# Performance work log

Measured on AMD Instinct MI355X. Metric: run time of the kernel, lower is better.

Reference implementation:

```python
import jax, jax.numpy as jnp
import numpy as np

B, T, C = 4, 2048, 1024
H = 16
HD = C // H  # 64


def setup_inputs() -> dict:
    key = jax.random.key(0)
    k1, k2, k3 = jax.random.split(key, 3)
    x = jax.random.normal(k1, (B, T, C), dtype=jnp.float32)
    W_attn = jax.random.normal(k2, (C, 3 * C), dtype=jnp.float32) * (1.0 / np.sqrt(C))
    b_attn = jnp.zeros((3 * C,), dtype=jnp.float32)
    W_proj = jax.random.normal(k3, (C, C), dtype=jnp.float32) * (1.0 / np.sqrt(C))
    b_proj = jnp.zeros((C,), dtype=jnp.float32)
    return {"x": x, "W_attn": W_attn, "b_attn": b_attn, "W_proj": W_proj, "b_proj": b_proj}


def reference(x, W_attn, b_attn, W_proj, b_proj):
    Bx, Tx, Cx = x.shape
    qkv = x @ W_attn + b_attn                      # [B,T,3C]
    q, k, v = jnp.split(qkv, 3, axis=-1)
    # [B,T,C] -> [B,H,T,HD]
    q = q.reshape(Bx, Tx, H, HD).transpose(0, 2, 1, 3)
    k = k.reshape(Bx, Tx, H, HD).transpose(0, 2, 1, 3)
    v = v.reshape(Bx, Tx, H, HD).transpose(0, 2, 1, 3)
    att = jnp.einsum('bhqd,bhkd->bhqk', q, k) / jnp.sqrt(jnp.float32(HD))
    causal = jnp.tril(jnp.ones((Tx, Tx), dtype=bool))
    att = jnp.where(causal[None, None], att, -jnp.inf)
    att = jax.nn.softmax(att, axis=-1)
    y = jnp.einsum('bhqk,bhkd->bhqd', att, v)      # [B,H,T,HD]
    y = y.transpose(0, 2, 1, 3).reshape(Bx, Tx, Cx)
    return y @ W_proj + b_proj
```

## Files before the change

kernel.cpp:

```cpp
#include <hip/hip_runtime.h>
#include <hip/hip_bf16.h>

typedef unsigned short u16;
typedef __attribute__((ext_vector_type(8))) short bf16x8;
typedef __attribute__((ext_vector_type(4))) float f32x4;

#define MFMA16(a, b, c) __builtin_amdgcn_mfma_f32_16x16x32_bf16((a), (b), (c), 0, 0, 0)

__device__ __forceinline__ u16 f2bf(float f) {
  union { float f; unsigned u; } v; v.f = f;
  unsigned r = v.u + 0x7fffu + ((v.u >> 16) & 1u);
  return (u16)(r >> 16);
}

__device__ __forceinline__ unsigned pk_trunc(float hi, float lo) {
  union { float f; unsigned u; } a, b; a.f = hi; b.f = lo;
  return __builtin_amdgcn_perm(a.u, b.u, 0x07060302u);
}

__device__ __forceinline__ void gload_lds16(const u16* g, u16* l) {
  __builtin_amdgcn_global_load_lds((const __attribute__((address_space(1))) void*)g,
                                   (__attribute__((address_space(3))) void*)l, 16, 0, 0);
}

__global__ __launch_bounds__(256) void convert_bf16_k(const float* __restrict__ in,
                                                      u16* __restrict__ out, int n) {
  int i = (blockIdx.x * 256 + threadIdx.x) * 4;
  if (i >= n) return;
  float4 v = *(const float4*)(in + i);
  ushort4 o;
  o.x = f2bf(v.x); o.y = f2bf(v.y); o.z = f2bf(v.z); o.w = f2bf(v.w);
  *(ushort4*)(out + i) = o;
}

__global__ __launch_bounds__(256) void transpose_bf16_k(const float* __restrict__ W,
                                                        u16* __restrict__ Wt, int K, int N) {
  __shared__ float tile[64][65];
  const int n0 = blockIdx.x * 64, k0 = blockIdx.y * 64;
  const int tx = threadIdx.x & 63, ty = threadIdx.x >> 6;
#pragma unroll
  for (int i = 0; i < 16; ++i)
    tile[ty + 4 * i][tx] = W[(size_t)(k0 + ty + 4 * i) * N + n0 + tx];
  __syncthreads();
#pragma unroll
  for (int i = 0; i < 16; ++i)
    Wt[(size_t)(n0 + ty + 4 * i) * K + k0 + tx] = f2bf(tile[tx][ty + 4 * i]);
}

#define GEMM_CORE(Aptr, Btptr)                                                     \
  __shared__ u16 As[128 * 32];                                                     \
  __shared__ u16 Bs[128 * 32];                                                     \
  const int m0 = blockIdx.y * 128, n0 = blockIdx.x * 128;                          \
  const int tid = threadIdx.x;                                                     \
  const int w = tid >> 6, lane = tid & 63;                                         \
  const int wm = w & 1, wn = w >> 1;                                               \
  const int fr = lane & 15, fg = lane >> 4;                                        \
  const int srow = lane >> 2, skof = (lane & 3) * 8;                               \
  const u16* gA0 = (Aptr) + (size_t)(m0 + w * 32 + srow) * 1024 + skof;            \
  const u16* gB0 = (Btptr) + (size_t)(n0 + w * 32 + srow) * 1024 + skof;           \
  u16* lA = As + w * 1024;                                                         \
  u16* lB = Bs + w * 1024;                                                         \
  f32x4 acc[4][4];                                                                 \
  _Pragma("unroll") for (int i = 0; i < 4; i++)                                    \
      _Pragma("unroll") for (int j = 0; j < 4; j++) acc[i][j] = (f32x4){0, 0, 0, 0}; \
  for (int kt = 0; kt < 32; ++kt) {                                                \
    const int ko = kt * 32;                                                        \
    gload_lds16(gA0 + ko, lA);                                                     \
    gload_lds16(gA0 + ko + 16 * 1024, lA + 512);                                   \
    gload_lds16(gB0 + ko, lB);                                                     \
    gload_lds16(gB0 + ko + 16 * 1024, lB + 512);                                   \
    __syncthreads();                                                               \
    bf16x8 af[4], bfr[4];                                                          \
    _Pragma("unroll") for (int mb = 0; mb < 4; ++mb)                               \
        af[mb] = *(const bf16x8*)&As[(wm * 64 + mb * 16 + fr) * 32 + fg * 8];      \
    _Pragma("unroll") for (int nb = 0; nb < 4; ++nb)                               \
        bfr[nb] = *(const bf16x8*)&Bs[(wn * 64 + nb * 16 + fr) * 32 + fg * 8];     \
    _Pragma("unroll") for (int mb = 0; mb < 4; ++mb)                               \
        _Pragma("unroll") for (int nb = 0; nb < 4; ++nb)                           \
            acc[mb][nb] = MFMA16(af[mb], bfr[nb], acc[mb][nb]);                    \
    __syncthreads();                                                               \
  }

__global__ __launch_bounds__(256) void gemm_qkv(const u16* __restrict__ A,
                                                const u16* __restrict__ Bt,
                                                const float* __restrict__ bias,
                                                u16* __restrict__ Qo, u16* __restrict__ Ko,
                                                u16* __restrict__ Vt) {
  GEMM_CORE(A, Bt)
  const int which = n0 >> 10;
#pragma unroll
  for (int nb = 0; nb < 4; ++nb) {
    const int n = n0 + wn * 64 + nb * 16 + fr;
    const float bs = bias[n];
    const int c = n & 1023, h = c >> 6, hd = c & 63;
#pragma unroll
    for (int mb = 0; mb < 4; ++mb) {
      const int mbase = m0 + wm * 64 + mb * 16 + fg * 4;
      const int bb = mbase >> 11;
      const int t = mbase & 2047;
      if (which == 0) {
        u16* dst = Qo + ((size_t)(bb * 16 + h) * 2048 + t) * 64 + hd;
#pragma unroll
        for (int r = 0; r < 4; ++r) dst[(size_t)r * 64] = f2bf((acc[mb][nb][r] + bs) * 0.125f);
      } else if (which == 1) {
        u16* dst = Ko + ((size_t)(bb * 16 + h) * 2048 + t) * 64 + hd;
#pragma unroll
        for (int r = 0; r < 4; ++r) dst[(size_t)r * 64] = f2bf(acc[mb][nb][r] + bs);
      } else {
        ushort4 pv;
        pv.x = f2bf(acc[mb][nb][0] + bs);
        pv.y = f2bf(acc[mb][nb][1] + bs);
        pv.z = f2bf(acc[mb][nb][2] + bs);
        pv.w = f2bf(acc[mb][nb][3] + bs);
        *(ushort4*)(Vt + ((size_t)(bb * 16 + h) * 64 + hd) * 2048 + t) = pv;
      }
    }
  }
}

__global__ __launch_bounds__(256) void gemm_proj(const u16* __restrict__ A,
                                                 const u16* __restrict__ Bt,
                                                 const float* __restrict__ bias,
                                                 float* __restrict__ O) {
  GEMM_CORE(A, Bt)
#pragma unroll
  for (int nb = 0; nb < 4; ++nb) {
    const int n = n0 + wn * 64 + nb * 16 + fr;
    const float bs = bias[n];
#pragma unroll
    for (int mb = 0; mb < 4; ++mb) {
#pragma unroll
      for (int r = 0; r < 4; ++r) {
        const int m = m0 + wm * 64 + mb * 16 + fg * 4 + r;
        O[(size_t)m * 1024 + n] = acc[mb][nb][r] + bs;
      }
    }
  }
}

#define PSTR 88
__global__ __launch_bounds__(256) void attn_k(const u16* __restrict__ Q,
                                              const u16* __restrict__ Kb,
                                              const u16* __restrict__ Vt,
                                              u16* __restrict__ Y) {
  __shared__ u16 Ks[64 * 72];
  __shared__ u16 Vs[64 * 72];
  __shared__ u16 Ps[4 * 32 * PSTR];
  const int L = blockIdx.x;
  const int xcd = L & 7, slot = L >> 3;
  const int bh = xcd * 8 + (slot & 7);
  const int qt = 15 - (slot >> 3);
  const int tid = threadIdx.x, w = tid >> 6, lane = tid & 63;
  const int fr = lane & 15, fg = lane >> 4;
  const u16* Qp = Q + (size_t)bh * 2048 * 64;
  const u16* Kp = Kb + (size_t)bh * 2048 * 64;
  const u16* Vp = Vt + (size_t)bh * 64 * 2048;
  const int qw = qt * 128 + w * 32;

  bf16x8 qa[2][2];
#pragma unroll
  for (int g = 0; g < 2; ++g)
#pragma unroll
    for (int c = 0; c < 2; ++c)
      qa[g][c] = *(const bf16x8*)(Qp + (size_t)(qw + g * 16 + fr) * 64 + c * 32 + fg * 8);

  float li[2] = {0.f, 0.f};
  f32x4 ot[2][4];
#pragma unroll
  for (int g = 0; g < 2; ++g)
#pragma unroll
    for (int mb = 0; mb < 4; ++mb) ot[g][mb] = (f32x4){0, 0, 0, 0};

  const int srow = tid >> 2, scol = (tid & 3) * 16;
  u16* Pw = Ps + w * 32 * PSTR;
  const int nk = 2 * qt + 2;
  const u16* Kg = Kp + (size_t)srow * 64 + scol;
  const u16* Vg = Vp + (size_t)srow * 2048 + scol;

  uint4 kr0 = *(const uint4*)(Kg);
  uint4 kr1 = *(const uint4*)(Kg + 8);
  uint4 vr0 = *(const uint4*)(Vg);
  uint4 vr1 = *(const uint4*)(Vg + 8);

  for (int jt = 0; jt < nk; ++jt) {
    const int k0 = jt * 64;
    if (jt) __syncthreads();
    *(uint4*)&Ks[srow * 72 + scol] = kr0;
    *(uint4*)&Ks[srow * 72 + scol + 8] = kr1;
    *(uint4*)&Vs[srow * 72 + scol] = vr0;
    *(uint4*)&Vs[srow * 72 + scol + 8] = vr1;
    __syncthreads();
    if (jt + 1 < nk) {
      const int kn = (jt + 1) * 64;
      kr0 = *(const uint4*)(Kg + (size_t)kn * 64);
      kr1 = *(const uint4*)(Kg + (size_t)kn * 64 + 8);
      vr0 = *(const uint4*)(Vg + kn);
      vr1 = *(const uint4*)(Vg + kn + 8);
    }
    if (k0 > qw + 31) continue;

    bf16x8 kb[4][2];
#pragma unroll
    for (int nb = 0; nb < 4; ++nb) {
      kb[nb][0] = *(const bf16x8*)&Ks[(nb * 16 + fr) * 72 + fg * 8];
      kb[nb][1] = *(const bf16x8*)&Ks[(nb * 16 + fr) * 72 + 32 + fg * 8];
    }
    f32x4 st[2][4];
#pragma unroll
    for (int g = 0; g < 2; ++g)
#pragma unroll
      for (int nb = 0; nb < 4; ++nb) {
        f32x4 z = (f32x4){0, 0, 0, 0};
        z = MFMA16(kb[nb][0], qa[g][0], z);
        z = MFMA16(kb[nb][1], qa[g][1], z);
        st[g][nb] = z;
      }
    const bool needmask = (k0 + 63 > qw);
#pragma unroll
    for (int g = 0; g < 2; ++g) {
      const int q = qw + g * 16 + fr;
      float rs0 = 0.f, rs1 = 0.f;
#pragma unroll
      for (int nb = 0; nb < 4; ++nb) {
        const int kcb = k0 + nb * 16 + 4 * fg;
        float p0 = __expf(st[g][nb][0]);
        float p1 = __expf(st[g][nb][1]);
        float p2 = __expf(st[g][nb][2]);
        float p3 = __expf(st[g][nb][3]);
        if (needmask) {
          p0 = (kcb + 0 > q) ? 0.f : p0;
          p1 = (kcb + 1 > q) ? 0.f : p1;
          p2 = (kcb + 2 > q) ? 0.f : p2;
          p3 = (kcb + 3 > q) ? 0.f : p3;
        }
        rs0 += p0 + p1;
        rs1 += p2 + p3;
        *(uint2*)&Pw[(g * 16 + fr) * PSTR + nb * 16 + 4 * fg] =
            make_uint2(pk_trunc(p1, p0), pk_trunc(p3, p2));
      }
      li[g] += rs0 + rs1;
    }
    bf16x8 pa[2][2];
#pragma unroll
    for (int g = 0; g < 2; ++g)
#pragma unroll
      for (int H = 0; H < 2; ++H)
        pa[g][H] = *(const bf16x8*)&Pw[(g * 16 + fr) * PSTR + H * 32 + fg * 8];
#pragma unroll
    for (int mb = 0; mb < 4; ++mb) {
      bf16x8 vb0 = *(const bf16x8*)&Vs[(mb * 16 + fr) * 72 + fg * 8];
      bf16x8 vb1 = *(const bf16x8*)&Vs[(mb * 16 + fr) * 72 + 32 + fg * 8];
#pragma unroll
      for (int g = 0; g < 2; ++g) {
        ot[g][mb] = MFMA16(vb0, pa[g][0], ot[g][mb]);
        ot[g][mb] = MFMA16(vb1, pa[g][1], ot[g][mb]);
      }
    }
  }

  const int b = bh >> 4, h = bh & 15;
#pragma unroll
  for (int g = 0; g < 2; ++g) {
    float l = li[g];
    l += __shfl_xor(l, 16);
    l += __shfl_xor(l, 32);
    const float inv = 1.0f / l;
    const int t = qw + g * 16 + fr;
    u16* yrow = Y + ((size_t)b * 2048 + t) * 1024 + h * 64;
#pragma unroll
    for (int mb = 0; mb < 4; ++mb) {
      const unsigned d0 = (unsigned)f2bf(ot[g][mb][0] * inv) |
                          ((unsigned)f2bf(ot[g][mb][1] * inv) << 16);
      const unsigned d1 = (unsigned)f2bf(ot[g][mb][2] * inv) |
                          ((unsigned)f2bf(ot[g][mb][3] * inv) << 16);
      *(uint2*)&yrow[mb * 16 + fg * 4] = make_uint2(d0, d1);
    }
  }
}

extern "C" void kernel_launch(void* const* d_in, const int* in_sizes, int n_in,
                              void* d_out, int out_size, void* d_ws, size_t ws_size,
                              hipStream_t stream) {
  const float* x = (const float*)d_in[0];
  const float* Wa = (const float*)d_in[1];
  const float* ba = (const float*)d_in[2];
  const float* Wp = (const float*)d_in[3];
  const float* bp = (const float*)d_in[4];
  float* out = (float*)d_out;

  char* p = (char*)d_ws;
  u16* xb = (u16*)p;   p += (size_t)8192 * 1024 * 2;
  u16* WaT = (u16*)p;  p += (size_t)3072 * 1024 * 2;
  u16* WpT = (u16*)p;  p += (size_t)1024 * 1024 * 2;
  u16* Qb = (u16*)p;   p += (size_t)64 * 2048 * 64 * 2;
  u16* Kbuf = (u16*)p; p += (size_t)64 * 2048 * 64 * 2;
  u16* Vtb = (u16*)p;  p += (size_t)64 * 64 * 2048 * 2;
  u16* Yb = (u16*)p;   p += (size_t)8192 * 1024 * 2;

  convert_bf16_k<<<8192, 256, 0, stream>>>(x, xb, 8192 * 1024);
  transpose_bf16_k<<<dim3(48, 16), 256, 0, stream>>>(Wa, WaT, 1024, 3072);
  transpose_bf16_k<<<dim3(16, 16), 256, 0, stream>>>(Wp, WpT, 1024, 1024);
  gemm_qkv<<<dim3(24, 64), 256, 0, stream>>>(xb, WaT, ba, Qb, Kbuf, Vtb);
  attn_k<<<1024, 256, 0, stream>>>(Qb, Kbuf, Vtb, Yb);
  gemm_proj<<<dim3(8, 64), 256, 0, stream>>>(Yb, WpT, bp, out);
}
```

Baseline: 270.9 us.

## Swap MFMA operands for row-vectorized GEMM epilogues, merge weight transposes, remap blocks

Merges the two weight-transpose launches into one kernel. Swaps the MFMA operand order in the Q/K and projection GEMMs so each lane holds four consecutive columns, which lets the epilogue write packed 8-byte bf16 or 16-byte float4 stores instead of scattered 2- or 4-byte stores. Remaps the 1D block index so consecutive blocks share an M tile and are spread across XCDs for better L2 reuse. It also changes the attention P-buffer stride from 88 to 72, which may introduce LDS bank conflicts.

```diff
diff --git a/kernel.cpp b/kernel.cpp
--- a/kernel.cpp
+++ b/kernel.cpp
@@ -33,10 +33,13 @@
   *(ushort4*)(out + i) = o;
 }
 
-__global__ __launch_bounds__(256) void transpose_bf16_k(const float* __restrict__ W,
-                                                        u16* __restrict__ Wt, int K, int N) {
+__global__ __launch_bounds__(256) void transpose2_k(const float* __restrict__ Wa, u16* __restrict__ WaT,
+                                                    const float* __restrict__ Wp, u16* __restrict__ WpT) {
   __shared__ float tile[64][65];
-  const int n0 = blockIdx.x * 64, k0 = blockIdx.y * 64;
+  int b = blockIdx.x;
+  const float* W; u16* Wt; int N, n0, k0;
+  if (b < 768) { W = Wa; Wt = WaT; N = 3072; n0 = (b % 48) * 64; k0 = (b / 48) * 64; }
+  else { int c = b - 768; W = Wp; Wt = WpT; N = 1024; n0 = (c & 15) * 64; k0 = (c >> 4) * 64; }
   const int tx = threadIdx.x & 63, ty = threadIdx.x >> 6;
 #pragma unroll
   for (int i = 0; i < 16; ++i)
@@ -44,41 +47,45 @@
   __syncthreads();
 #pragma unroll
   for (int i = 0; i < 16; ++i)
-    Wt[(size_t)(n0 + ty + 4 * i) * K + k0 + tx] = f2bf(tile[tx][ty + 4 * i]);
-}
-
-#define GEMM_CORE(Aptr, Btptr)                                                     \
+    Wt[(size_t)(n0 + ty + 4 * i) * 1024 + k0 + tx] = f2bf(tile[tx][ty + 4 * i]);
+}
+
+#define GEMM_PROLOG                                                                \
   __shared__ u16 As[128 * 32];                                                     \
   __shared__ u16 Bs[128 * 32];                                                     \
-  const int m0 = blockIdx.y * 128, n0 = blockIdx.x * 128;                          \
   const int tid = threadIdx.x;                                                     \
   const int w = tid >> 6, lane = tid & 63;                                         \
   const int wm = w & 1, wn = w >> 1;                                               \
   const int fr = lane & 15, fg = lane >> 4;                                        \
   const int srow = lane >> 2, skof = (lane & 3) * 8;                               \
-  const u16* gA0 = (Aptr) + (size_t)(m0 + w * 32 + srow) * 1024 + skof;            \
-  const u16* gB0 = (Btptr) + (size_t)(n0 + w * 32 + srow) * 1024 + skof;           \
   u16* lA = As + w * 1024;                                                         \
   u16* lB = Bs + w * 1024;                                                         \
   f32x4 acc[4][4];                                                                 \
   _Pragma("unroll") for (int i = 0; i < 4; i++)                                    \
-      _Pragma("unroll") for (int j = 0; j < 4; j++) acc[i][j] = (f32x4){0, 0, 0, 0}; \
-  for (int kt = 0; kt < 32; ++kt) {                                                \
-    const int ko = kt * 32;                                                        \
-    gload_lds16(gA0 + ko, lA);                                                     \
-    gload_lds16(gA0 + ko + 16 * 1024, lA + 512);                                   \
-    gload_lds16(gB0 + ko, lB);                                                     \
-    gload_lds16(gB0 + ko + 16 * 1024, lB + 512);                                   \
-    __syncthreads();                                                               \
-    bf16x8 af[4], bfr[4];                                                          \
-    _Pragma("unroll") for (int mb = 0; mb < 4; ++mb)                               \
-        af[mb] = *(const bf16x8*)&As[(wm * 64 + mb * 16 + fr) * 32 + fg * 8];      \
-    _Pragma("unroll") for (int nb = 0; nb < 4; ++nb)                               \
-        bfr[nb] = *(const bf16x8*)&Bs[(wn * 64 + nb * 16 + fr) * 32 + fg * 8];     \
-    _Pragma("unroll") for (int mb = 0; mb < 4; ++mb)                               \
-        _Pragma("unroll") for (int nb = 0; nb < 4; ++nb)                           \
-            acc[mb][nb] = MFMA16(af[mb], bfr[nb], acc[mb][nb]);                    \
-    __syncthreads();                                                               \
+      _Pragma("unroll") for (int j = 0; j < 4; j++) acc[i][j] = (f32x4){0, 0, 0, 0};
+
+#define GEMM_KLOOP(Aptr, Btptr, SWAP)                                              \
+  {                                                                                \
+    const u16* gA0 = (Aptr) + (size_t)(m0 + w * 32 + srow) * 1024 + skof;          \
+    const u16* gB0 = (Btptr) + (size_t)(n0 + w * 32 + srow) * 1024 + skof;         \
+    for (int kt = 0; kt < 32; ++kt) {                                              \
+      const int ko = kt * 32;                                                      \
+      gload_lds16(gA0 + ko, lA);                                                   \
+      gload_lds16(gA0 + ko + 16 * 1024, lA + 512);                                 \
+      gload_lds16(gB0 + ko, lB);                                                   \
+      gload_lds16(gB0 + ko + 16 * 1024, lB + 512);                                 \
+      __syncthreads();                                                             \
+      bf16x8 af[4], bfr[4];                                                        \
+      _Pragma("unroll") for (int mb = 0; mb < 4; ++mb)                             \
+          af[mb] = *(const bf16x8*)&As[(wm * 64 + mb * 16 + fr) * 32 + fg * 8];    \
+      _Pragma("unroll") for (int nb = 0; nb < 4; ++nb)                             \
+          bfr[nb] = *(const bf16x8*)&Bs[(wn * 64 + nb * 16 + fr) * 32 + fg * 8];   \
+      _Pragma("unroll") for (int mb = 0; mb < 4; ++mb)                             \
+          _Pragma("unroll") for (int nb = 0; nb < 4; ++nb)                         \
+              acc[mb][nb] = (SWAP) ? MFMA16(bfr[nb], af[mb], acc[mb][nb])          \
+                                   : MFMA16(af[mb], bfr[nb], acc[mb][nb]);         \
+      __syncthreads();                                                             \
+    }                                                                              \
   }
 
 __global__ __launch_bounds__(256) void gemm_qkv(const u16* __restrict__ A,
@@ -86,27 +93,46 @@
                                                 const float* __restrict__ bias,
                                                 u16* __restrict__ Qo, u16* __restrict__ Ko,
                                                 u16* __restrict__ Vt) {
-  GEMM_CORE(A, Bt)
+  const int id = blockIdx.x;
+  const int s = id >> 3;
+  const int nt = (id & 7) * 3 + s % 3;
+  const int mt = s / 3;
+  const int m0 = mt * 128, n0 = nt * 128;
+  GEMM_PROLOG
   const int which = n0 >> 10;
-#pragma unroll
-  for (int nb = 0; nb < 4; ++nb) {
-    const int n = n0 + wn * 64 + nb * 16 + fr;
-    const float bs = bias[n];
-    const int c = n & 1023, h = c >> 6, hd = c & 63;
+  if (which < 2) {
+    GEMM_KLOOP(A, Bt, 1)
+    const float sc = (which == 0) ? 0.125f : 1.0f;
+    u16* Out = (which == 0) ? Qo : Ko;
 #pragma unroll
     for (int mb = 0; mb < 4; ++mb) {
-      const int mbase = m0 + wm * 64 + mb * 16 + fg * 4;
-      const int bb = mbase >> 11;
-      const int t = mbase & 2047;
-      if (which == 0) {
-        u16* dst = Qo + ((size_t)(bb * 16 + h) * 2048 + t) * 64 + hd;
-#pragma unroll
-        for (int r = 0; r < 4; ++r) dst[(size_t)r * 64] = f2bf((acc[mb][nb][r] + bs) * 0.125f);
-      } else if (which == 1) {
-        u16* dst = Ko + ((size_t)(bb * 16 + h) * 2048 + t) * 64 + hd;
-#pragma unroll
-        for (int r = 0; r < 4; ++r) dst[(size_t)r * 64] = f2bf(acc[mb][nb][r] + bs);
-      } else {
+      const int tg = m0 + wm * 64 + mb * 16 + fr;
+      const int bb = tg >> 11, t = tg & 2047;
+#pragma unroll
+      for (int nb = 0; nb < 4; ++nb) {
+        const int n = n0 + wn * 64 + nb * 16 + 4 * fg;
+        const float4 b4 = *(const float4*)(bias + n);
+        const int c = n & 1023, h = c >> 6, d0 = c & 63;
+        const float v0 = (acc[mb][nb][0] + b4.x) * sc;
+        const float v1 = (acc[mb][nb][1] + b4.y) * sc;
+        const float v2 = (acc[mb][nb][2] + b4.z) * sc;
+        const float v3 = (acc[mb][nb][3] + b4.w) * sc;
+        const unsigned lo = (unsigned)f2bf(v0) | ((unsigned)f2bf(v1) << 16);
+        const unsigned hi = (unsigned)f2bf(v2) | ((unsigned)f2bf(v3) << 16);
+        *(uint2*)(Out + ((size_t)(bb * 16 + h) * 2048 + t) * 64 + d0) = make_uint2(lo, hi);
+      }
+    }
+  } else {
+    GEMM_KLOOP(A, Bt, 0)
+#pragma unroll
+    for (int nb = 0; nb < 4; ++nb) {
+      const int n = n0 + wn * 64 + nb * 16 + fr;
+      const float bs = bias[n];
+      const int c = n & 1023, h = c >> 6, hd = c & 63;
+#pragma unroll
+      for (int mb = 0; mb < 4; ++mb) {
+        const int mbase = m0 + wm * 64 + mb * 16 + fg * 4;
+        const int bb = mbase >> 11, t = mbase & 2047;
         ushort4 pv;
         pv.x = f2bf(acc[mb][nb][0] + bs);
         pv.y = f2bf(acc[mb][nb][1] + bs);
@@ -122,23 +148,28 @@
                                                  const u16* __restrict__ Bt,
                                                  const float* __restrict__ bias,
                                                  float* __restrict__ O) {
-  GEMM_CORE(A, Bt)
-#pragma unroll
-  for (int nb = 0; nb < 4; ++nb) {
-    const int n = n0 + wn * 64 + nb * 16 + fr;
-    const float bs = bias[n];
-#pragma unroll
-    for (int mb = 0; mb < 4; ++mb) {
-#pragma unroll
-      for (int r = 0; r < 4; ++r) {
-        const int m = m0 + wm * 64 + mb * 16 + fg * 4 + r;
-        O[(size_t)m * 1024 + n] = acc[mb][nb][r] + bs;
-      }
-    }
-  }
-}
-
-#define PSTR 88
+  const int id = blockIdx.x;
+  const int m0 = (id >> 3) * 128, n0 = (id & 7) * 128;
+  GEMM_PROLOG
+  GEMM_KLOOP(A, Bt, 1)
+#pragma unroll
+  for (int mb = 0; mb < 4; ++mb) {
+    const int tg = m0 + wm * 64 + mb * 16 + fr;
+#pragma unroll
+    for (int nb = 0; nb < 4; ++nb) {
+      const int n = n0 + wn * 64 + nb * 16 + 4 * fg;
+      const float4 b4 = *(const float4*)(bias + n);
+      float4 o;
+      o.x = acc[mb][nb][0] + b4.x;
+      o.y = acc[mb][nb][1] + b4.y;
+      o.z = acc[mb][nb][2] + b4.z;
+      o.w = acc[mb][nb][3] + b4.w;
+      *(float4*)(O + (size_t)tg * 1024 + n) = o;
+    }
+  }
+}
+
+#define PSTR 72
 __global__ __launch_bounds__(256) void attn_k(const u16* __restrict__ Q,
                                               const u16* __restrict__ Kb,
                                               const u16* __restrict__ Vt,
@@ -298,9 +329,8 @@
   u16* Yb = (u16*)p;   p += (size_t)8192 * 1024 * 2;
 
   convert_bf16_k<<<8192, 256, 0, stream>>>(x, xb, 8192 * 1024);
-  transpose_bf16_k<<<dim3(48, 16), 256, 0, stream>>>(Wa, WaT, 1024, 3072);
-  transpose_bf16_k<<<dim3(16, 16), 256, 0, stream>>>(Wp, WpT, 1024, 1024);
-  gemm_qkv<<<dim3(24, 64), 256, 0, stream>>>(xb, WaT, ba, Qb, Kbuf, Vtb);
+  transpose2_k<<<1024, 256, 0, stream>>>(Wa, WaT, Wp, WpT);
+  gemm_qkv<<<1536, 256, 0, stream>>>(xb, WaT, ba, Qb, Kbuf, Vtb);
   attn_k<<<1024, 256, 0, stream>>>(Qb, Kbuf, Vtb, Yb);
-  gemm_proj<<<dim3(8, 64), 256, 0, stream>>>(Yb, WpT, bp, out);
-}
+  gemm_proj<<<512, 256, 0, stream>>>(Yb, WpT, bp, out);
+}
```

Measured after the change: 271.7 us. No clear change (+0.3%).
